# Kernel optimization log

Measured on AMD Instinct MI355X. Metric: run time of the kernel, lower is better.

Reference implementation:

```python
import jax, jax.numpy as jnp
import numpy as np
from jax import lax

INPUT_DIM = 512
KERNEL_DIM = 3
HEADS = 8
B, L = 16, 1024


def setup_inputs() -> dict:
    key = jax.random.key(0)
    ks = jax.random.split(key, 4)
    fan = INPUT_DIM * KERNEL_DIM
    std = float(np.sqrt(2.0 / (INPUT_DIM + fan)))  # xavier_normal for conv weight
    x = jax.random.normal(ks[0], (B, INPUT_DIM, L), dtype=jnp.float32)
    w0 = jax.random.normal(ks[1], (INPUT_DIM, INPUT_DIM, KERNEL_DIM), dtype=jnp.float32) * std
    w1 = jax.random.normal(ks[2], (INPUT_DIM, INPUT_DIM, KERNEL_DIM), dtype=jnp.float32) * std
    w2 = jax.random.normal(ks[3], (INPUT_DIM, INPUT_DIM, KERNEL_DIM), dtype=jnp.float32) * std
    b0 = jnp.zeros((INPUT_DIM,), jnp.float32)
    b1 = jnp.zeros((INPUT_DIM,), jnp.float32)
    b2 = jnp.zeros((INPUT_DIM,), jnp.float32)
    return {"x": x, "w0": w0, "b0": b0, "w1": w1, "b1": b1, "w2": w2, "b2": b2}


def _conv1d(x, w, b):
    # x: [B, C, L], w: [O, I, K] -> [B, O, L-K+1] (VALID, stride 1)
    y = lax.conv_general_dilated(x, w, window_strides=(1,), padding='VALID',
                                 dimension_numbers=('NCH', 'OIH', 'NCH'))
    return y + b[None, :, None]


def _multihead_attention(q, k, v, input_dim, heads):
    # q,k,v: [B, D, Lp]; chunk along channel dim == reshape to [B, H, Dh, Lp]
    b, d, lp = q.shape
    dh = d // heads
    qh = q.reshape(b, heads, dh, lp)
    kh = k.reshape(b, heads, dh, lp)
    vh = v.reshape(b, heads, dh, lp)
    scale = 1.0 / np.sqrt(input_dim)  # NOTE: original scales by sqrt(full input_dim)
    scores = jnp.einsum('bhdq,bhdk->bhqk', qh, kh) * scale  # [B,H,Lp,Lp]
    attn = jax.nn.softmax(scores, axis=-1)
    out = jnp.einsum('bhqk,bhdk->bhdq', attn, vh)  # [B,H,Dh,Lp]
    return out.reshape(b, d, lp)


def reference(x, w0, b0, w1, b1, w2, b2):
    q = _conv1d(x, w0, b0)
    k = _conv1d(x, w1, b1)
    v = _conv1d(x, w2, b2)
    return _multihead_attention(q, k, v, INPUT_DIM, HEADS)
```

## Files before the change

### kernel.cpp

```cpp
#include <hip/hip_runtime.h>

#define B_SZ 16
#define CIN  512
#define LIN  1024
#define LP   1022
#define HEADS 8
#define DH    64

typedef __attribute__((ext_vector_type(8))) short bf16x8;
typedef __attribute__((ext_vector_type(4))) float f32x4;

__device__ inline unsigned short f2bf(float f) {
    union { float f; unsigned int u; } c; c.f = f;
    unsigned int r = c.u + 0x7FFF + ((c.u >> 16) & 1);
    return (unsigned short)(r >> 16);
}

__device__ __forceinline__ void gl_lds16(const unsigned short* g, unsigned short* l) {
    __builtin_amdgcn_global_load_lds((const __attribute__((address_space(1))) void*)g,
                                     (__attribute__((address_space(3))) void*)l, 16, 0, 0);
}

#define SWZ(G) ((G) ^ (((G) >> 3) & 7))

__global__ __launch_bounds__(256) void xb_cvt_kernel(const float* __restrict__ x,
                                                     unsigned short* __restrict__ xb) {
    __shared__ float sm[64][68];
    const int t  = threadIdx.x;
    const int l0 = blockIdx.x * 64;
    const int i0 = blockIdx.y * 64;
    const int b  = blockIdx.z;
    const float* S = x + ((size_t)b * CIN + i0) * LIN;

    #pragma unroll
    for (int rr = 0; rr < 4; rr++) {
        int idx = rr * 1024 + t * 4;
        int ii = idx >> 6, lj = idx & 63;
        *(float4*)&sm[ii][lj] = *(const float4*)(S + (size_t)ii * LIN + l0 + lj);
    }
    __syncthreads();

    #pragma unroll
    for (int rr = 0; rr < 4; rr++) {
        int idx = rr * 1024 + t * 4;
        int l = idx >> 6, dj = idx & 63;
        ushort4 h;
        h.x = f2bf(sm[dj + 0][l]);
        h.y = f2bf(sm[dj + 1][l]);
        h.z = f2bf(sm[dj + 2][l]);
        h.w = f2bf(sm[dj + 3][l]);
        *(ushort4*)(xb + ((size_t)b * 1024 + l0 + l) * 512 + i0 + dj) = h;
    }
}

__global__ __launch_bounds__(256) void wb_cvt_kernel(const float* __restrict__ w0,
                                                     const float* __restrict__ w1,
                                                     const float* __restrict__ w2,
                                                     unsigned short* __restrict__ wb) {
    const int kk = blockIdx.y;
    int flat = blockIdx.x * 256 + threadIdx.x;
    int i  = flat & 511;
    int oG = flat >> 9;
    int c  = oG >> 9, o = oG & 511;
    const float* w = (c == 0) ? w0 : (c == 1) ? w1 : w2;
    wb[(size_t)kk * 786432 + flat] = f2bf(w[o * 1536 + i * 3 + kk]);
}

__global__ __launch_bounds__(256) void conv_mfma_kernel(
        const unsigned short* __restrict__ xb,
        const unsigned short* __restrict__ wb,
        const float* __restrict__ b0, const float* __restrict__ b1,
        const float* __restrict__ b2,
        unsigned short* __restrict__ Qt, unsigned short* __restrict__ Kt,
        unsigned short* __restrict__ Vt, float qscale) {
    __shared__ unsigned short smem[16896];
    unsigned short* xs = smem;
    unsigned short* ws = smem + 4224;

    const int t    = threadIdx.x;
    const int wave = t >> 6;
    const int lane = t & 63;
    const int col  = lane & 15;
    const int quad = lane >> 4;
    const int wh   = wave >> 1;
    const int wn   = wave & 1;
    const int l0   = blockIdx.x * 128;
    const int o0   = blockIdx.y * 128;
    const int b    = blockIdx.z;

    f32x4 acc[4][4];
    #pragma unroll
    for (int i = 0; i < 4; i++)
        #pragma unroll
        for (int j = 0; j < 4; j++) acc[i][j] = (f32x4){0.f, 0.f, 0.f, 0.f};

    const unsigned short* xrow = xb + (size_t)b * 1024 * 512;

    for (int ic = 0; ic < 512; ic += 32) {
        __syncthreads();

        #pragma unroll
        for (int j = 0; j < 6; j++) {
            int instr = wave * 6 + j;
            int Gg = SWZ(instr * 64 + lane);
            int p = Gg >> 2, q = Gg & 3;
            int kk = p >> 7, orow = p & 127;
            gl_lds16(wb + ((size_t)(kk * 1536 + o0 + orow)) * 512 + ic + q * 8,
                     ws + instr * 512);
        }
        #pragma unroll
        for (int j = 0; j < 2; j++) {
            int instr = wave * 2 + j;
            int Gg = SWZ(instr * 64 + lane);
            int p = Gg >> 2, q = Gg & 3;
            gl_lds16(xrow + (size_t)(l0 + p) * 512 + ic + q * 8,
                     xs + instr * 512);
        }
        if (t < 8) {
            int row = 128 + (t >> 2), sg = t & 3;
            int gl = l0 + row;
            bf16x8 v = (bf16x8){0, 0, 0, 0, 0, 0, 0, 0};
            if (gl < 1024) v = *(const bf16x8*)(xrow + (size_t)gl * 512 + ic + sg * 8);
            *(bf16x8*)&xs[SWZ(512 + t) * 8] = v;
        }
        __syncthreads();

        #pragma unroll
        for (int kk = 0; kk < 3; kk++) {
            bf16x8 af[4], bfr[4];
            #pragma unroll
            for (int ms = 0; ms < 4; ms++) {
                int G = ((kk * 128 + wh * 64 + ms * 16 + col) << 2) | quad;
                af[ms] = *(const bf16x8*)&ws[SWZ(G) * 8];
            }
            #pragma unroll
            for (int ns = 0; ns < 4; ns++) {
                int G = ((wn * 64 + ns * 16 + col + kk) << 2) | quad;
                bfr[ns] = *(const bf16x8*)&xs[SWZ(G) * 8];
            }
            #pragma unroll
            for (int ms = 0; ms < 4; ms++)
                #pragma unroll
                for (int ns = 0; ns < 4; ns++)
                    acc[ms][ns] = __builtin_amdgcn_mfma_f32_16x16x32_bf16(af[ms], bfr[ns], acc[ms][ns], 0, 0, 0);
        }
    }

    const int c = blockIdx.y >> 2;

    if (c < 2) {
        unsigned short* dst = (c == 0) ? Qt : Kt;
        const float* bias   = (c == 0) ? b0 : b1;
        const float sc      = (c == 0) ? qscale : 1.0f;
        const int h = (((o0 & 511) + wh * 64) >> 6) & 7;
        unsigned short* base = dst + (size_t)(b * 8 + h) * 65536;
        #pragma unroll
        for (int ms = 0; ms < 4; ms++) {
            int ob = (o0 & 511) + wh * 64 + ms * 16 + quad * 4;
            float bv[4];
            #pragma unroll
            for (int r = 0; r < 4; r++) bv[r] = bias[ob + r];
            int d0 = ms * 16 + quad * 4;
            #pragma unroll
            for (int ns = 0; ns < 4; ns++) {
                int l = l0 + wn * 64 + ns * 16 + col;
                ushort4 hv;
                hv.x = f2bf((acc[ms][ns][0] + bv[0]) * sc);
                hv.y = f2bf((acc[ms][ns][1] + bv[1]) * sc);
                hv.z = f2bf((acc[ms][ns][2] + bv[2]) * sc);
                hv.w = f2bf((acc[ms][ns][3] + bv[3]) * sc);
                *(ushort4*)(base + (size_t)l * 64 + d0) = hv;
            }
        }
    } else {
        __syncthreads();
        unsigned short* vt = smem;
        #pragma unroll
        for (int ms = 0; ms < 4; ms++) {
            int ob = (o0 & 511) + wh * 64 + ms * 16 + quad * 4;
            #pragma unroll
            for (int ns = 0; ns < 4; ns++) {
                int lc = wn * 64 + ns * 16 + col;
                #pragma unroll
                for (int r = 0; r < 4; r++)
                    vt[(wh * 64 + ms * 16 + quad * 4 + r) * 132 + lc] =
                        f2bf(acc[ms][ns][r] + b2[ob + r]);
            }
        }
        __syncthreads();
        #pragma unroll
        for (int it = 0; it < 8; it++) {
            int flat = it * 2048 + t * 8;
            int row = flat >> 7, colx = flat & 127;
            bf16x8 v = *(const bf16x8*)&vt[row * 132 + colx];
            int og = (o0 & 511) + row;
            int h = og >> 6, d = og & 63;
            *(bf16x8*)(Vt + ((size_t)(b * 8 + h) * 64 + d) * 1024 + l0 + colx) = v;
        }
    }
}

__global__ __launch_bounds__(256, 3) void attn_kernel(
        const unsigned short* __restrict__ Qt,
        const unsigned short* __restrict__ Kt,
        const unsigned short* __restrict__ Vt,
        float* __restrict__ out) {
    __shared__ unsigned short smem[25600];
    unsigned short* Ps = smem + 16384;

    const int t    = threadIdx.x;
    const int wave = t >> 6;
    const int lane = t & 63;
    const int col  = lane & 15;
    const int quad = lane >> 4;

    const int lin = blockIdx.y * 8 + blockIdx.x;
    const int xcd = lin & 7;
    const int idx = lin >> 3;
    const int qb  = idx >> 4;
    const int bh  = xcd * 16 + (idx & 15);

    const size_t base64 = (size_t)bh * 1024 * 64;
    const int q0w = qb * 128 + wave * 32;

    bf16x8 bq[2][2];
    #pragma unroll
    for (int g = 0; g < 2; g++) {
        const unsigned short* qrow = Qt + base64 + (size_t)(q0w + g * 16 + col) * 64;
        bq[g][0] = *(const bf16x8*)(qrow + quad * 8);
        bq[g][1] = *(const bf16x8*)(qrow + 32 + quad * 8);
    }

    const bf16x8 ones = (bf16x8){0x3F80, 0x3F80, 0x3F80, 0x3F80,
                                 0x3F80, 0x3F80, 0x3F80, 0x3F80};

    f32x4 o[2][4];
    #pragma unroll
    for (int g = 0; g < 2; g++)
        #pragma unroll
        for (int d = 0; d < 4; d++) o[g][d] = (f32x4){0.f, 0.f, 0.f, 0.f};
    f32x4 osum[2];
    osum[0] = (f32x4){0.f, 0.f, 0.f, 0.f};
    osum[1] = (f32x4){0.f, 0.f, 0.f, 0.f};

    const unsigned short* kg0 = Kt + base64;
    const unsigned short* vg  = Vt + base64;
    unsigned short* Pw = Ps + wave * 32 * 72;

    #pragma unroll
    for (int j = 0; j < 2; j++) {
        int i = wave + j * 4;
        int G = SWZ(i * 64 + lane);
        gl_lds16(kg0 + (size_t)G * 8, smem + i * 512);
        int p = G >> 3, q = G & 7;
        gl_lds16(vg + (size_t)p * 1024 + q * 8, smem + 4096 + i * 512);
    }
    asm volatile("s_waitcnt vmcnt(0)" ::: "memory");
    __builtin_amdgcn_s_barrier();
    asm volatile("" ::: "memory");

    int cur = 0;
    for (int kt = 0; kt < 16; kt++) {
        if (kt < 15) {
            const unsigned short* kg = kg0 + (size_t)(kt + 1) * 4096;
            unsigned short* Kb = smem + (cur ^ 1) * 8192;
            #pragma unroll
            for (int j = 0; j < 2; j++) {
                int i = wave + j * 4;
                int G = SWZ(i * 64 + lane);
                gl_lds16(kg + (size_t)G * 8, Kb + i * 512);
                int p = G >> 3, q = G & 7;
                gl_lds16(vg + (size_t)p * 1024 + (kt + 1) * 64 + q * 8,
                         Kb + 4096 + i * 512);
            }
        }

        const unsigned short* Ksb = smem + cur * 8192;
        const unsigned short* Vsb = Ksb + 4096;

        bf16x8 ak[4][2];
        #pragma unroll
        for (int sub = 0; sub < 4; sub++) {
            int rk = sub * 16 + col;
            ak[sub][0] = *(const bf16x8*)&Ksb[SWZ(rk * 8 + quad) * 8];
            ak[sub][1] = *(const bf16x8*)&Ksb[SWZ(rk * 8 + 4 + quad) * 8];
        }
        bf16x8 av[4][2];
        #pragma unroll
        for (int dsub = 0; dsub < 4; dsub++) {
            int rd = dsub * 16 + col;
            av[dsub][0] = *(const bf16x8*)&Vsb[SWZ(rd * 8 + quad) * 8];
            av[dsub][1] = *(const bf16x8*)&Vsb[SWZ(rd * 8 + 4 + quad) * 8];
        }

        #pragma unroll
        for (int g = 0; g < 2; g++) {
            #pragma unroll
            for (int sub = 0; sub < 4; sub++) {
                f32x4 a = (f32x4){0.f, 0.f, 0.f, 0.f};
                __builtin_amdgcn_s_setprio(1);
                a = __builtin_amdgcn_mfma_f32_16x16x32_bf16(ak[sub][0], bq[g][0], a, 0, 0, 0);
                a = __builtin_amdgcn_mfma_f32_16x16x32_bf16(ak[sub][1], bq[g][1], a, 0, 0, 0);
                __builtin_amdgcn_s_setprio(0);
                unsigned int u[4];
                #pragma unroll
                for (int r = 0; r < 4; r++) {
                    union { float f; unsigned int u; } c;
                    c.f = exp2f(a[r]);
                    u[r] = c.u;
                }
                if (kt == 15 && sub == 3 && quad == 3) {
                    u[2] = 0; u[3] = 0;
                }
                uint2 pk;
                pk.x = (u[0] >> 16) | (u[1] & 0xFFFF0000u);
                pk.y = (u[2] >> 16) | (u[3] & 0xFFFF0000u);
                *(uint2*)&Pw[(g * 16 + col) * 72 + sub * 16 + quad * 4] = pk;
            }
        }

        #pragma unroll
        for (int g = 0; g < 2; g++) {
            bf16x8 bp0 = *(const bf16x8*)&Pw[(g * 16 + col) * 72 + quad * 8];
            bf16x8 bp1 = *(const bf16x8*)&Pw[(g * 16 + col) * 72 + 32 + quad * 8];
            __builtin_amdgcn_s_setprio(1);
            #pragma unroll
            for (int dsub = 0; dsub < 4; dsub++) {
                o[g][dsub] = __builtin_amdgcn_mfma_f32_16x16x32_bf16(av[dsub][0], bp0, o[g][dsub], 0, 0, 0);
                o[g][dsub] = __builtin_amdgcn_mfma_f32_16x16x32_bf16(av[dsub][1], bp1, o[g][dsub], 0, 0, 0);
            }
            osum[g] = __builtin_amdgcn_mfma_f32_16x16x32_bf16(ones, bp0, osum[g], 0, 0, 0);
            osum[g] = __builtin_amdgcn_mfma_f32_16x16x32_bf16(ones, bp1, osum[g], 0, 0, 0);
            __builtin_amdgcn_s_setprio(0);
        }

        asm volatile("s_waitcnt vmcnt(0)" ::: "memory");
        __builtin_amdgcn_s_barrier();
        asm volatile("" ::: "memory");
        cur ^= 1;
    }

    #pragma unroll
    for (int g = 0; g < 2; g++) {
        int q = q0w + g * 16 + col;
        if (q < LP) {
            float inv = 1.0f / osum[g][0];
            #pragma unroll
            for (int dsub = 0; dsub < 4; dsub++) {
                #pragma unroll
                for (int r = 0; r < 4; r++) {
                    int d = dsub * 16 + quad * 4 + r;
                    out[((size_t)bh * 64 + d) * LP + q] = o[g][dsub][r] * inv;
                }
            }
        }
    }
}

extern "C" void kernel_launch(void* const* d_in, const int* in_sizes, int n_in,
                              void* d_out, int out_size, void* d_ws, size_t ws_size,
                              hipStream_t stream) {
    const float* x  = (const float*)d_in[0];
    const float* w0 = (const float*)d_in[1];
    const float* b0 = (const float*)d_in[2];
    const float* w1 = (const float*)d_in[3];
    const float* b1 = (const float*)d_in[4];
    const float* w2 = (const float*)d_in[5];
    const float* b2 = (const float*)d_in[6];
    float* out = (float*)d_out;

    unsigned short* xbp = (unsigned short*)d_ws;
    unsigned short* wbp = xbp + 8388608;
    unsigned short* Qt  = wbp + 2359296;
    unsigned short* Kt  = Qt + 8388608;
    unsigned short* Vt  = Kt + 8388608;

    const float scale = 0.06375870864f;

    xb_cvt_kernel<<<dim3(16, 8, 16), 256, 0, stream>>>(x, xbp);
    wb_cvt_kernel<<<dim3(3072, 3), 256, 0, stream>>>(w0, w1, w2, wbp);
    conv_mfma_kernel<<<dim3(8, 12, 16), 256, 0, stream>>>(xbp, wbp, b0, b1, b2,
                                                          Qt, Kt, Vt, scale);
    attn_kernel<<<dim3(8, 128), 256, 0, stream>>>(Qt, Kt, Vt, out);
}
```

Before: 242.3 us.

## Rewrite conv GEMM with 256x128 tiles and triple-buffered async LDS pipeline

The conv kernel moves to 512 threads with a 256x128 output tile and iterates over 24 K-tiles (3 taps x 8 channel chunks). Each tile's weight and input chunks are staged into triple-buffered dynamic LDS with global_load_lds, two tiles ahead. Fragment loads are interleaved with MFMA groups, using barriers and s_setprio, so global loads overlap compute instead of the previous load-sync-compute loop. The block needs 144KB of dynamic LDS, which limits occupancy to one block per CU. The input loads for the last L tile can now read past the valid rows, where the old code zero-padded them.

```diff
diff --git a/kernel.cpp b/kernel.cpp
--- a/kernel.cpp
+++ b/kernel.cpp
@@ -22,6 +22,10 @@
 }
 
 #define SWZ(G) ((G) ^ (((G) >> 3) & 7))
+
+#define BAR() do { asm volatile("" ::: "memory"); \
+                   __builtin_amdgcn_s_barrier();  \
+                   asm volatile("" ::: "memory"); } while (0)
 
 __global__ __launch_bounds__(256) void xb_cvt_kernel(const float* __restrict__ x,
                                                      unsigned short* __restrict__ xb) {
@@ -66,28 +70,143 @@
     wb[(size_t)kk * 786432 + flat] = f2bf(w[o * 1536 + i * 3 + kk]);
 }
 
-__global__ __launch_bounds__(256) void conv_mfma_kernel(
+extern __shared__ unsigned short smem[];
+
+__device__ __forceinline__ void stage_chunkA(const unsigned short* wbase,
+                                             unsigned short* bufA, int wave, int lane) {
+    #pragma unroll
+    for (int j = 0; j < 2; j++) {
+        int i = wave * 2 + j;
+        int G = SWZ(i * 64 + lane);
+        gl_lds16(wbase + (size_t)(G >> 3) * 512 + (G & 7) * 8, bufA + i * 512);
+    }
+}
+
+__device__ __forceinline__ void stage_chunkB(const unsigned short* xbase,
+                                             unsigned short* bufB, int half,
+                                             int wave, int lane) {
+    #pragma unroll
+    for (int j = 0; j < 2; j++) {
+        int i = half * 16 + wave * 2 + j;
+        int G = SWZ(i * 64 + lane);
+        gl_lds16(xbase + (size_t)(G >> 3) * 512 + (G & 7) * 8, bufB + i * 512);
+    }
+}
+
+__device__ __forceinline__ bf16x8 ldfrag(const unsigned short* buf, int row,
+                                         int ks, int quad) {
+    int G = (row << 3) | (ks << 2) | quad;
+    return *(const bf16x8*)&buf[SWZ(G) * 8];
+}
+
+__device__ __forceinline__ void ktile(int kt,
+        const unsigned short* __restrict__ wb, const unsigned short* __restrict__ xrow,
+        int o0, int l0, int wave, int lane, int col, int quad, int wr, int wc,
+        unsigned short* BA, unsigned short* BB,
+        unsigned short* NA, unsigned short* NB, f32x4 (&acc)[4][4]) {
+    const int kn  = kt + 2;
+    const int kkn = kn >> 3, icn = (kn & 7) << 6;
+    const int ar = wr * 64 + col;
+    const int br = wc * 64 + col;
+
+    bf16x8 A0[2][2], A1[2][2], Bl[2][2], Bh[2][2];
+
+    if (kt < 22)
+        stage_chunkA(wb + (size_t)kkn * 786432 + (size_t)o0 * 512 + icn, NA, wave, lane);
+    #pragma unroll
+    for (int ks = 0; ks < 2; ks++) {
+        A0[0][ks] = ldfrag(BA, ar,      ks, quad);
+        A0[1][ks] = ldfrag(BA, ar + 16, ks, quad);
+        Bl[0][ks] = ldfrag(BB, br,      ks, quad);
+        Bl[1][ks] = ldfrag(BB, br + 16, ks, quad);
+    }
+    BAR();
+    __builtin_amdgcn_s_setprio(1);
+    #pragma unroll
+    for (int ks = 0; ks < 2; ks++) {
+        acc[0][0] = __builtin_amdgcn_mfma_f32_16x16x32_bf16(A0[0][ks], Bl[0][ks], acc[0][0], 0, 0, 0);
+        acc[0][1] = __builtin_amdgcn_mfma_f32_16x16x32_bf16(A0[0][ks], Bl[1][ks], acc[0][1], 0, 0, 0);
+        acc[1][0] = __builtin_amdgcn_mfma_f32_16x16x32_bf16(A0[1][ks], Bl[0][ks], acc[1][0], 0, 0, 0);
+        acc[1][1] = __builtin_amdgcn_mfma_f32_16x16x32_bf16(A0[1][ks], Bl[1][ks], acc[1][1], 0, 0, 0);
+    }
+    __builtin_amdgcn_s_setprio(0);
+    BAR();
+
+    if (kt < 22)
+        stage_chunkB(xrow + (size_t)(l0 + kkn) * 512 + icn, NB, 0, wave, lane);
+    #pragma unroll
+    for (int ks = 0; ks < 2; ks++) {
+        Bh[0][ks] = ldfrag(BB, br + 32, ks, quad);
+        Bh[1][ks] = ldfrag(BB, br + 48, ks, quad);
+    }
+    BAR();
+    __builtin_amdgcn_s_setprio(1);
+    #pragma unroll
+    for (int ks = 0; ks < 2; ks++) {
+        acc[0][2] = __builtin_amdgcn_mfma_f32_16x16x32_bf16(A0[0][ks], Bh[0][ks], acc[0][2], 0, 0, 0);
+        acc[0][3] = __builtin_amdgcn_mfma_f32_16x16x32_bf16(A0[0][ks], Bh[1][ks], acc[0][3], 0, 0, 0);
+        acc[1][2] = __builtin_amdgcn_mfma_f32_16x16x32_bf16(A0[1][ks], Bh[0][ks], acc[1][2], 0, 0, 0);
+        acc[1][3] = __builtin_amdgcn_mfma_f32_16x16x32_bf16(A0[1][ks], Bh[1][ks], acc[1][3], 0, 0, 0);
+    }
+    __builtin_amdgcn_s_setprio(0);
+    BAR();
+
+    if (kt < 22)
+        stage_chunkB(xrow + (size_t)(l0 + kkn) * 512 + icn, NB, 1, wave, lane);
+    #pragma unroll
+    for (int ks = 0; ks < 2; ks++) {
+        A1[0][ks] = ldfrag(BA, ar + 32, ks, quad);
+        A1[1][ks] = ldfrag(BA, ar + 48, ks, quad);
+    }
+    BAR();
+    __builtin_amdgcn_s_setprio(1);
+    #pragma unroll
+    for (int ks = 0; ks < 2; ks++) {
+        acc[2][2] = __builtin_amdgcn_mfma_f32_16x16x32_bf16(A1[0][ks], Bh[0][ks], acc[2][2], 0, 0, 0);
+        acc[2][3] = __builtin_amdgcn_mfma_f32_16x16x32_bf16(A1[0][ks], Bh[1][ks], acc[2][3], 0, 0, 0);
+        acc[3][2] = __builtin_amdgcn_mfma_f32_16x16x32_bf16(A1[1][ks], Bh[0][ks], acc[3][2], 0, 0, 0);
+        acc[3][3] = __builtin_amdgcn_mfma_f32_16x16x32_bf16(A1[1][ks], Bh[1][ks], acc[3][3], 0, 0, 0);
+    }
+    __builtin_amdgcn_s_setprio(0);
+    BAR();
+
+    __builtin_amdgcn_s_setprio(1);
+    #pragma unroll
+    for (int ks = 0; ks < 2; ks++) {
+        acc[2][0] = __builtin_amdgcn_mfma_f32_16x16x32_bf16(A1[0][ks], Bl[0][ks], acc[2][0], 0, 0, 0);
+        acc[2][1] = __builtin_amdgcn_mfma_f32_16x16x32_bf16(A1[0][ks], Bl[1][ks], acc[2][1], 0, 0, 0);
+        acc[3][0] = __builtin_amdgcn_mfma_f32_16x16x32_bf16(A1[1][ks], Bl[0][ks], acc[3][0], 0, 0, 0);
+        acc[3][1] = __builtin_amdgcn_mfma_f32_16x16x32_bf16(A1[1][ks], Bl[1][ks], acc[3][1], 0, 0, 0);
+    }
+    __builtin_amdgcn_s_setprio(0);
+
+    if (kt < 22)       asm volatile("s_waitcnt vmcnt(6)" ::: "memory");
+    else if (kt == 22) asm volatile("s_waitcnt vmcnt(0)" ::: "memory");
+    BAR();
+}
+
+__global__ __launch_bounds__(512, 2) void conv_mfma_kernel(
         const unsigned short* __restrict__ xb,
         const unsigned short* __restrict__ wb,
         const float* __restrict__ b0, const float* __restrict__ b1,
         const float* __restrict__ b2,
         unsigned short* __restrict__ Qt, unsigned short* __restrict__ Kt,
         unsigned short* __restrict__ Vt, float qscale) {
-    __shared__ unsigned short smem[16896];
-    unsigned short* xs = smem;
-    unsigned short* ws = smem + 4224;
-
     const int t    = threadIdx.x;
     const int wave = t >> 6;
     const int lane = t & 63;
     const int col  = lane & 15;
     const int quad = lane >> 4;
-    const int wh   = wave >> 1;
-    const int wn   = wave & 1;
-    const int l0   = blockIdx.x * 128;
+    const int wr   = wave >> 2;
+    const int wc   = wave & 3;
+    const int l0   = blockIdx.x * 256;
     const int o0   = blockIdx.y * 128;
     const int b    = blockIdx.z;
 
+    unsigned short* b0A = smem;          unsigned short* b0B = smem + 8192;
+    unsigned short* b1A = smem + 24576;  unsigned short* b1B = smem + 32768;
+    unsigned short* b2A = smem + 49152;  unsigned short* b2B = smem + 57344;
+
     f32x4 acc[4][4];
     #pragma unroll
     for (int i = 0; i < 4; i++)
@@ -96,54 +215,23 @@
 
     const unsigned short* xrow = xb + (size_t)b * 1024 * 512;
 
-    for (int ic = 0; ic < 512; ic += 32) {
-        __syncthreads();
-
-        #pragma unroll
-        for (int j = 0; j < 6; j++) {
-            int instr = wave * 6 + j;
-            int Gg = SWZ(instr * 64 + lane);
-            int p = Gg >> 2, q = Gg & 3;
-            int kk = p >> 7, orow = p & 127;
-            gl_lds16(wb + ((size_t)(kk * 1536 + o0 + orow)) * 512 + ic + q * 8,
-                     ws + instr * 512);
-        }
-        #pragma unroll
-        for (int j = 0; j < 2; j++) {
-            int instr = wave * 2 + j;
-            int Gg = SWZ(instr * 64 + lane);
-            int p = Gg >> 2, q = Gg & 3;
-            gl_lds16(xrow + (size_t)(l0 + p) * 512 + ic + q * 8,
-                     xs + instr * 512);
-        }
-        if (t < 8) {
-            int row = 128 + (t >> 2), sg = t & 3;
-            int gl = l0 + row;
-            bf16x8 v = (bf16x8){0, 0, 0, 0, 0, 0, 0, 0};
-            if (gl < 1024) v = *(const bf16x8*)(xrow + (size_t)gl * 512 + ic + sg * 8);
-            *(bf16x8*)&xs[SWZ(512 + t) * 8] = v;
-        }
-        __syncthreads();
-
-        #pragma unroll
-        for (int kk = 0; kk < 3; kk++) {
-            bf16x8 af[4], bfr[4];
-            #pragma unroll
-            for (int ms = 0; ms < 4; ms++) {
-                int G = ((kk * 128 + wh * 64 + ms * 16 + col) << 2) | quad;
-                af[ms] = *(const bf16x8*)&ws[SWZ(G) * 8];
-            }
-            #pragma unroll
-            for (int ns = 0; ns < 4; ns++) {
-                int G = ((wn * 64 + ns * 16 + col + kk) << 2) | quad;
-                bfr[ns] = *(const bf16x8*)&xs[SWZ(G) * 8];
-            }
-            #pragma unroll
-            for (int ms = 0; ms < 4; ms++)
-                #pragma unroll
-                for (int ns = 0; ns < 4; ns++)
-                    acc[ms][ns] = __builtin_amdgcn_mfma_f32_16x16x32_bf16(af[ms], bfr[ns], acc[ms][ns], 0, 0, 0);
-        }
+    stage_chunkA(wb + (size_t)o0 * 512,        b0A, wave, lane);
+    stage_chunkB(xrow + (size_t)l0 * 512,      b0B, 0, wave, lane);
+    stage_chunkB(xrow + (size_t)l0 * 512,      b0B, 1, wave, lane);
+    stage_chunkA(wb + (size_t)o0 * 512 + 64,   b1A, wave, lane);
+    stage_chunkB(xrow + (size_t)l0 * 512 + 64, b1B, 0, wave, lane);
+    stage_chunkB(xrow + (size_t)l0 * 512 + 64, b1B, 1, wave, lane);
+    asm volatile("s_waitcnt vmcnt(6)" ::: "memory");
+    BAR();
+
+    #pragma unroll 1
+    for (int ktb = 0; ktb < 24; ktb += 3) {
+        ktile(ktb,     wb, xrow, o0, l0, wave, lane, col, quad, wr, wc,
+              b0A, b0B, b2A, b2B, acc);
+        ktile(ktb + 1, wb, xrow, o0, l0, wave, lane, col, quad, wr, wc,
+              b1A, b1B, b0A, b0B, acc);
+        ktile(ktb + 2, wb, xrow, o0, l0, wave, lane, col, quad, wr, wc,
+              b2A, b2B, b1A, b1B, acc);
     }
 
     const int c = blockIdx.y >> 2;
@@ -152,18 +240,19 @@
         unsigned short* dst = (c == 0) ? Qt : Kt;
         const float* bias   = (c == 0) ? b0 : b1;
         const float sc      = (c == 0) ? qscale : 1.0f;
-        const int h = (((o0 & 511) + wh * 64) >> 6) & 7;
+        const int obase = (o0 & 511) + wr * 64;
+        const int h = obase >> 6;
         unsigned short* base = dst + (size_t)(b * 8 + h) * 65536;
         #pragma unroll
         for (int ms = 0; ms < 4; ms++) {
-            int ob = (o0 & 511) + wh * 64 + ms * 16 + quad * 4;
+            int ob = obase + ms * 16 + quad * 4;
             float bv[4];
             #pragma unroll
             for (int r = 0; r < 4; r++) bv[r] = bias[ob + r];
             int d0 = ms * 16 + quad * 4;
             #pragma unroll
             for (int ns = 0; ns < 4; ns++) {
-                int l = l0 + wn * 64 + ns * 16 + col;
+                int l = l0 + wc * 64 + ns * 16 + col;
                 ushort4 hv;
                 hv.x = f2bf((acc[ms][ns][0] + bv[0]) * sc);
                 hv.y = f2bf((acc[ms][ns][1] + bv[1]) * sc);
@@ -177,22 +266,22 @@
         unsigned short* vt = smem;
         #pragma unroll
         for (int ms = 0; ms < 4; ms++) {
-            int ob = (o0 & 511) + wh * 64 + ms * 16 + quad * 4;
+            int ob = (o0 & 511) + wr * 64 + ms * 16 + quad * 4;
             #pragma unroll
             for (int ns = 0; ns < 4; ns++) {
-                int lc = wn * 64 + ns * 16 + col;
+                int lc = wc * 64 + ns * 16 + col;
                 #pragma unroll
                 for (int r = 0; r < 4; r++)
-                    vt[(wh * 64 + ms * 16 + quad * 4 + r) * 132 + lc] =
+                    vt[(wr * 64 + ms * 16 + quad * 4 + r) * 264 + lc] =
                         f2bf(acc[ms][ns][r] + b2[ob + r]);
             }
         }
         __syncthreads();
         #pragma unroll
         for (int it = 0; it < 8; it++) {
-            int flat = it * 2048 + t * 8;
-            int row = flat >> 7, colx = flat & 127;
-            bf16x8 v = *(const bf16x8*)&vt[row * 132 + colx];
+            int flat = it * 4096 + t * 8;
+            int row = flat >> 8, colx = flat & 255;
+            bf16x8 v = *(const bf16x8*)&vt[row * 264 + colx];
             int og = (o0 & 511) + row;
             int h = og >> 6, d = og & 63;
             *(bf16x8*)(Vt + ((size_t)(b * 8 + h) * 64 + d) * 1024 + l0 + colx) = v;
@@ -205,8 +294,8 @@
         const unsigned short* __restrict__ Kt,
         const unsigned short* __restrict__ Vt,
         float* __restrict__ out) {
-    __shared__ unsigned short smem[25600];
-    unsigned short* Ps = smem + 16384;
+    __shared__ unsigned short asmem[25600];
+    unsigned short* Ps = asmem + 16384;
 
     const int t    = threadIdx.x;
     const int wave = t >> 6;
@@ -251,9 +340,9 @@
     for (int j = 0; j < 2; j++) {
         int i = wave + j * 4;
         int G = SWZ(i * 64 + lane);
-        gl_lds16(kg0 + (size_t)G * 8, smem + i * 512);
+        gl_lds16(kg0 + (size_t)G * 8, asmem + i * 512);
         int p = G >> 3, q = G & 7;
-        gl_lds16(vg + (size_t)p * 1024 + q * 8, smem + 4096 + i * 512);
+        gl_lds16(vg + (size_t)p * 1024 + q * 8, asmem + 4096 + i * 512);
     }
     asm volatile("s_waitcnt vmcnt(0)" ::: "memory");
     __builtin_amdgcn_s_barrier();
@@ -263,7 +352,7 @@
     for (int kt = 0; kt < 16; kt++) {
         if (kt < 15) {
             const unsigned short* kg = kg0 + (size_t)(kt + 1) * 4096;
-            unsigned short* Kb = smem + (cur ^ 1) * 8192;
+            unsigned short* Kb = asmem + (cur ^ 1) * 8192;
             #pragma unroll
             for (int j = 0; j < 2; j++) {
                 int i = wave + j * 4;
@@ -275,7 +364,7 @@
             }
         }
 
-        const unsigned short* Ksb = smem + cur * 8192;
+        const unsigned short* Ksb = asmem + cur * 8192;
         const unsigned short* Vsb = Ksb + 4096;
 
         bf16x8 ak[4][2];
@@ -377,9 +466,16 @@
 
     const float scale = 0.06375870864f;
 
+    static bool attr_done = false;
+    if (!attr_done) {
+        hipFuncSetAttribute((const void*)conv_mfma_kernel,
+                            hipFuncAttributeMaxDynamicSharedMemorySize, 147456);
+        attr_done = true;
+    }
+
     xb_cvt_kernel<<<dim3(16, 8, 16), 256, 0, stream>>>(x, xbp);
     wb_cvt_kernel<<<dim3(3072, 3), 256, 0, stream>>>(w0, w1, w2, wbp);
-    conv_mfma_kernel<<<dim3(8, 12, 16), 256, 0, stream>>>(xbp, wbp, b0, b1, b2,
-                                                          Qt, Kt, Vt, scale);
+    conv_mfma_kernel<<<dim3(4, 12, 16), 512, 147456, stream>>>(xbp, wbp, b0, b1, b2,
+                                                               Qt, Kt, Vt, scale);
     attn_kernel<<<dim3(8, 128), 256, 0, stream>>>(Qt, Kt, Vt, out);
 }
```

After: 253.5 us. +4.6%, slower.

## Double attention query tile per block and use packed bf16 convert

Applied to the files above, without the earlier changes.

Each attention wave now handles 64 queries instead of 32, so a block covers 256 queries and the grid halves. This reuses each K/V tile staged in LDS across twice as many queries, reducing global and LDS traffic per unit of work. The bf16 packing of exp values now uses v_cvt_pk_bf16_f32 (round-to-nearest) instead of truncation via bit shifts, and the V fragment loads move after the P computation to lower register pressure. In exchange, register and LDS use grow, occupancy drops to 2 blocks per SIMD group, and the grid has fewer blocks.

```diff
diff --git a/kernel.cpp b/kernel.cpp
--- a/kernel.cpp
+++ b/kernel.cpp
@@ -200,13 +200,13 @@
     }
 }
 
-__global__ __launch_bounds__(256, 3) void attn_kernel(
+__global__ __launch_bounds__(256, 2) void attn_kernel(
         const unsigned short* __restrict__ Qt,
         const unsigned short* __restrict__ Kt,
         const unsigned short* __restrict__ Vt,
         float* __restrict__ out) {
-    __shared__ unsigned short smem[25600];
-    unsigned short* Ps = smem + 16384;
+    __shared__ unsigned short asmem[34816];
+    unsigned short* Ps = asmem + 16384;
 
     const int t    = threadIdx.x;
     const int wave = t >> 6;
@@ -214,18 +214,18 @@
     const int col  = lane & 15;
     const int quad = lane >> 4;
 
-    const int lin = blockIdx.y * 8 + blockIdx.x;
+    const int lin = blockIdx.y * 4 + blockIdx.x;
     const int xcd = lin & 7;
     const int idx = lin >> 3;
     const int qb  = idx >> 4;
     const int bh  = xcd * 16 + (idx & 15);
 
     const size_t base64 = (size_t)bh * 1024 * 64;
-    const int q0w = qb * 128 + wave * 32;
-
-    bf16x8 bq[2][2];
-    #pragma unroll
-    for (int g = 0; g < 2; g++) {
+    const int q0w = qb * 256 + wave * 64;
+
+    bf16x8 bq[4][2];
+    #pragma unroll
+    for (int g = 0; g < 4; g++) {
         const unsigned short* qrow = Qt + base64 + (size_t)(q0w + g * 16 + col) * 64;
         bq[g][0] = *(const bf16x8*)(qrow + quad * 8);
         bq[g][1] = *(const bf16x8*)(qrow + 32 + quad * 8);
@@ -234,26 +234,26 @@
     const bf16x8 ones = (bf16x8){0x3F80, 0x3F80, 0x3F80, 0x3F80,
                                  0x3F80, 0x3F80, 0x3F80, 0x3F80};
 
-    f32x4 o[2][4];
-    #pragma unroll
-    for (int g = 0; g < 2; g++)
+    f32x4 o[4][4];
+    #pragma unroll
+    for (int g = 0; g < 4; g++)
         #pragma unroll
         for (int d = 0; d < 4; d++) o[g][d] = (f32x4){0.f, 0.f, 0.f, 0.f};
-    f32x4 osum[2];
-    osum[0] = (f32x4){0.f, 0.f, 0.f, 0.f};
-    osum[1] = (f32x4){0.f, 0.f, 0.f, 0.f};
+    f32x4 osum[4];
+    #pragma unroll
+    for (int g = 0; g < 4; g++) osum[g] = (f32x4){0.f, 0.f, 0.f, 0.f};
 
     const unsigned short* kg0 = Kt + base64;
     const unsigned short* vg  = Vt + base64;
-    unsigned short* Pw = Ps + wave * 32 * 72;
+    unsigned short* Pw = Ps + wave * 64 * 72;
 
     #pragma unroll
     for (int j = 0; j < 2; j++) {
         int i = wave + j * 4;
         int G = SWZ(i * 64 + lane);
-        gl_lds16(kg0 + (size_t)G * 8, smem + i * 512);
+        gl_lds16(kg0 + (size_t)G * 8, asmem + i * 512);
         int p = G >> 3, q = G & 7;
-        gl_lds16(vg + (size_t)p * 1024 + q * 8, smem + 4096 + i * 512);
+        gl_lds16(vg + (size_t)p * 1024 + q * 8, asmem + 4096 + i * 512);
     }
     asm volatile("s_waitcnt vmcnt(0)" ::: "memory");
     __builtin_amdgcn_s_barrier();
@@ -263,7 +263,7 @@
     for (int kt = 0; kt < 16; kt++) {
         if (kt < 15) {
             const unsigned short* kg = kg0 + (size_t)(kt + 1) * 4096;
-            unsigned short* Kb = smem + (cur ^ 1) * 8192;
+            unsigned short* Kb = asmem + (cur ^ 1) * 8192;
             #pragma unroll
             for (int j = 0; j < 2; j++) {
                 int i = wave + j * 4;
@@ -275,7 +275,7 @@
             }
         }
 
-        const unsigned short* Ksb = smem + cur * 8192;
+        const unsigned short* Ksb = asmem + cur * 8192;
         const unsigned short* Vsb = Ksb + 4096;
 
         bf16x8 ak[4][2];
@@ -285,16 +285,9 @@
             ak[sub][0] = *(const bf16x8*)&Ksb[SWZ(rk * 8 + quad) * 8];
             ak[sub][1] = *(const bf16x8*)&Ksb[SWZ(rk * 8 + 4 + quad) * 8];
         }
-        bf16x8 av[4][2];
-        #pragma unroll
-        for (int dsub = 0; dsub < 4; dsub++) {
-            int rd = dsub * 16 + col;
-            av[dsub][0] = *(const bf16x8*)&Vsb[SWZ(rd * 8 + quad) * 8];
-            av[dsub][1] = *(const bf16x8*)&Vsb[SWZ(rd * 8 + 4 + quad) * 8];
-        }
-
-        #pragma unroll
-        for (int g = 0; g < 2; g++) {
+
+        #pragma unroll
+        for (int g = 0; g < 4; g++) {
             #pragma unroll
             for (int sub = 0; sub < 4; sub++) {
                 f32x4 a = (f32x4){0.f, 0.f, 0.f, 0.f};
@@ -302,25 +295,27 @@
                 a = __builtin_amdgcn_mfma_f32_16x16x32_bf16(ak[sub][0], bq[g][0], a, 0, 0, 0);
                 a = __builtin_amdgcn_mfma_f32_16x16x32_bf16(ak[sub][1], bq[g][1], a, 0, 0, 0);
                 __builtin_amdgcn_s_setprio(0);
-                unsigned int u[4];
-                #pragma unroll
-                for (int r = 0; r < 4; r++) {
-                    union { float f; unsigned int u; } c;
-                    c.f = exp2f(a[r]);
-                    u[r] = c.u;
-                }
-                if (kt == 15 && sub == 3 && quad == 3) {
-                    u[2] = 0; u[3] = 0;
-                }
+                float e0 = exp2f(a[0]), e1 = exp2f(a[1]);
+                float e2 = exp2f(a[2]), e3 = exp2f(a[3]);
                 uint2 pk;
-                pk.x = (u[0] >> 16) | (u[1] & 0xFFFF0000u);
-                pk.y = (u[2] >> 16) | (u[3] & 0xFFFF0000u);
+                asm("v_cvt_pk_bf16_f32 %0, %1, %2" : "=v"(pk.x) : "v"(e0), "v"(e1));
+                asm("v_cvt_pk_bf16_f32 %0, %1, %2" : "=v"(pk.y) : "v"(e2), "v"(e3));
+                if (kt == 15 && sub == 3 && quad == 3)
+                    pk.y = 0;
                 *(uint2*)&Pw[(g * 16 + col) * 72 + sub * 16 + quad * 4] = pk;
             }
         }
 
-        #pragma unroll
-        for (int g = 0; g < 2; g++) {
+        bf16x8 av[4][2];
+        #pragma unroll
+        for (int dsub = 0; dsub < 4; dsub++) {
+            int rd = dsub * 16 + col;
+            av[dsub][0] = *(const bf16x8*)&Vsb[SWZ(rd * 8 + quad) * 8];
+            av[dsub][1] = *(const bf16x8*)&Vsb[SWZ(rd * 8 + 4 + quad) * 8];
+        }
+
+        #pragma unroll
+        for (int g = 0; g < 4; g++) {
             bf16x8 bp0 = *(const bf16x8*)&Pw[(g * 16 + col) * 72 + quad * 8];
             bf16x8 bp1 = *(const bf16x8*)&Pw[(g * 16 + col) * 72 + 32 + quad * 8];
             __builtin_amdgcn_s_setprio(1);
@@ -341,7 +336,7 @@
     }
 
     #pragma unroll
-    for (int g = 0; g < 2; g++) {
+    for (int g = 0; g < 4; g++) {
         int q = q0w + g * 16 + col;
         if (q < LP) {
             float inv = 1.0f / osum[g][0];
@@ -381,5 +376,5 @@
     wb_cvt_kernel<<<dim3(3072, 3), 256, 0, stream>>>(w0, w1, w2, wbp);
     conv_mfma_kernel<<<dim3(8, 12, 16), 256, 0, stream>>>(xbp, wbp, b0, b1, b2,
                                                           Qt, Kt, Vt, scale);
-    attn_kernel<<<dim3(8, 128), 256, 0, stream>>>(Qt, Kt, Vt, out);
-}
+    attn_kernel<<<dim3(4, 128), 256, 0, stream>>>(Qt, Kt, Vt, out);
+}
```

After: 239.4 us. No clear change (-1.2%).
